# Kernel optimization log

Hardware: AMD Instinct MI355X
Metric: run time of the kernel (lower is better)

Reference implementation:

```python
import jax, jax.numpy as jnp
import numpy as np

B, S, D, H = 2, 2048, 1024, 16
DK = D // H


def setup_inputs() -> dict:
    key = jax.random.key(0)
    ks = jax.random.split(key, 12)
    k_init = 1.0 / np.sqrt(D)  # torch Linear-style uniform bound used in the module
    def lin(kw, kb):
        W = jax.random.uniform(kw, (D, D), jnp.float32, -k_init, k_init)
        b = jax.random.uniform(kb, (D,), jnp.float32, -k_init, k_init)
        return W, b
    Wq, bq = lin(ks[0], ks[1])
    Wk, bk = lin(ks[2], ks[3])
    Wv, bv = lin(ks[4], ks[5])
    Wo, bo = lin(ks[6], ks[7])
    query = jax.random.normal(ks[8], (B, S, D), jnp.float32)
    key_t = jax.random.normal(ks[9], (B, S, D), jnp.float32)
    value = jax.random.normal(ks[10], (B, S, D), jnp.float32)
    # causal mask: 1 where attention allowed, 0 where blocked
    mask = jnp.broadcast_to(jnp.tril(jnp.ones((S, S), jnp.int32)), (B, S, S))
    return {"query": query, "key": key_t, "value": value, "mask": mask,
            "Wq": Wq, "bq": bq, "Wk": Wk, "bk": bk, "Wv": Wv, "bv": bv,
            "Wo": Wo, "bo": bo}


def reference(query, key, value, mask, Wq, bq, Wk, bk, Wv, bv, Wo, bo):
    bs = query.shape[0]
    # projections: torch Linear computes x @ W.T + b
    def proj(x, W, b):
        y = x @ W.T + b                      # [B, S, D]
        return y.reshape(bs, -1, H, DK).transpose(0, 2, 1, 3)  # [B, H, S, DK]
    q = proj(query, Wq, bq)
    k = proj(key, Wk, bk)
    v = proj(value, Wv, bv)
    scale = 1.0 / np.sqrt(DK).astype(np.float32)
    scores = jnp.einsum('bhqd,bhkd->bhqk', q, k) * scale  # [B, H, S, S]
    scores = jnp.where(mask[:, None, :, :] == 0, jnp.float32(-1e9), scores)
    p_attn = jax.nn.softmax(scores, axis=-1)
    # dropout omitted (eval mode / deterministic reference)
    x = jnp.einsum('bhqk,bhkd->bhqd', p_attn, v)          # [B, H, S, DK]
    x = x.transpose(0, 2, 1, 3).reshape(bs, -1, D)        # [B, S, D]
    return x @ Wo.T + bo
```

## Files before the change

### kernel.cpp

```cpp
#include <hip/hip_runtime.h>
#include <hip/hip_bf16.h>
#include <math.h>

#define BB 2
#define SS 2048
#define DD 1024
#define HH 16
#define DKK 64
#define NT (BB * SS)

typedef __attribute__((ext_vector_type(8))) short short8;
typedef __attribute__((ext_vector_type(4))) short short4v;
typedef __attribute__((ext_vector_type(4))) float f32x4;

#define SWZ(r) ((((r) >> 3) ^ (r)) & 7)

__device__ __forceinline__ unsigned short f2b(float x) {
    __hip_bfloat16 h = __float2bfloat16(x);
    unsigned short u; __builtin_memcpy(&u, &h, 2); return u;
}

__device__ __forceinline__ f32x4 zero4() {
    f32x4 z; z[0] = 0.f; z[1] = 0.f; z[2] = 0.f; z[3] = 0.f; return z;
}

struct CastAll {
    const float* src[7];
    unsigned short* dst[7];
};

__global__ __launch_bounds__(256)
void cast_all(CastAll a) {
    const int tid0 = blockIdx.x * 256 + threadIdx.x;
    const int stride = gridDim.x * 256;
    #pragma unroll
    for (int s = 0; s < 7; ++s) {
        const int n4 = (s < 3) ? (NT * DD / 4) : (DD * DD / 4);
        const float* __restrict__ src = a.src[s];
        unsigned short* __restrict__ dst = a.dst[s];
        for (int i = tid0; i < n4; i += stride) {
            const float4 v = reinterpret_cast<const float4*>(src)[i];
            ushort4 o;
            o.x = f2b(v.x); o.y = f2b(v.y); o.z = f2b(v.z); o.w = f2b(v.w);
            reinterpret_cast<ushort4*>(dst)[i] = o;
        }
    }
}

template <typename OutT>
__device__ __forceinline__ void gemm_body(const unsigned short* __restrict__ A,
                                          const unsigned short* __restrict__ W,
                                          const float* __restrict__ bias,
                                          OutT* __restrict__ C,
                                          int bm, int bn, int N, int K) {
    __shared__ __align__(16) unsigned char sA[128 * 128];
    __shared__ __align__(16) unsigned char sB[128 * 128];

    const int tid = threadIdx.x;
    const int l = tid & 63;
    const int w = tid >> 6;
    const int wr = w >> 1, wc = w & 1;
    const int g = l >> 4, li = l & 15;
    const int lrow = l >> 3;
    const int lcol = (l & 7) * 8;

    f32x4 acc[4][4];
    #pragma unroll
    for (int i = 0; i < 4; ++i)
        #pragma unroll
        for (int jj = 0; jj < 4; ++jj) acc[i][jj] = zero4();

    for (int kt = 0; kt < K; kt += 64) {
        #pragma unroll
        for (int c = 0; c < 4; ++c) {
            const int row0 = w * 32 + c * 8;
            const unsigned short* gA = A + (size_t)(bm + row0 + lrow) * K + kt + lcol;
            __builtin_amdgcn_global_load_lds(
                (const __attribute__((address_space(1))) unsigned int*)gA,
                (__attribute__((address_space(3))) unsigned int*)&sA[row0 * 128],
                16, 0, 0);
            const unsigned short* gB = W + (size_t)(bn + row0 + lrow) * K + kt + lcol;
            __builtin_amdgcn_global_load_lds(
                (const __attribute__((address_space(1))) unsigned int*)gB,
                (__attribute__((address_space(3))) unsigned int*)&sB[row0 * 128],
                16, 0, 0);
        }
        __syncthreads();

        #pragma unroll
        for (int kb = 0; kb < 2; ++kb) {
            const int chb = (g + kb * 4) * 16;
            short8 af[4], bfr[4];
            #pragma unroll
            for (int mi = 0; mi < 4; ++mi)
                af[mi] = *reinterpret_cast<const short8*>(
                    &sA[(wr * 64 + mi * 16 + li) * 128 + chb]);
            #pragma unroll
            for (int ni = 0; ni < 4; ++ni)
                bfr[ni] = *reinterpret_cast<const short8*>(
                    &sB[(wc * 64 + ni * 16 + li) * 128 + chb]);
            #pragma unroll
            for (int mi = 0; mi < 4; ++mi)
                #pragma unroll
                for (int ni = 0; ni < 4; ++ni)
                    acc[mi][ni] = __builtin_amdgcn_mfma_f32_16x16x32_bf16(af[mi], bfr[ni], acc[mi][ni], 0, 0, 0);
        }
        __syncthreads();
    }

    #pragma unroll
    for (int ni = 0; ni < 4; ++ni) {
        const int col = bn + wc * 64 + ni * 16 + li;
        const float bv = bias[col];
        #pragma unroll
        for (int mi = 0; mi < 4; ++mi) {
            const int row0 = bm + wr * 64 + mi * 16 + g * 4;
            #pragma unroll
            for (int r = 0; r < 4; ++r) {
                const float v = acc[mi][ni][r] + bv;
                if constexpr (sizeof(OutT) == 2)
                    C[(size_t)(row0 + r) * N + col] = (OutT)f2b(v);
                else
                    C[(size_t)(row0 + r) * N + col] = (OutT)v;
            }
        }
    }
}

struct QKVArgs {
    const unsigned short* A[3];
    const unsigned short* W[3];
    const float* bias[3];
    unsigned short* C[3];
};

__global__ __launch_bounds__(256)
void gemm_qkv(QKVArgs args) {
    const int bid = blockIdx.x;
    const int i = (bid & 7) * 96 + (bid >> 3);
    const int z = i >> 8;
    const int rem = i & 255;
    const int by = rem >> 3, bx = rem & 7;
    gemm_body<unsigned short>(args.A[z], args.W[z], args.bias[z], args.C[z],
                              by * 128, bx * 128, DD, DD);
}

__global__ __launch_bounds__(256)
void gemm_out(const unsigned short* __restrict__ A, const unsigned short* __restrict__ W,
              const float* __restrict__ bias, float* __restrict__ C) {
    const int bid = blockIdx.x;
    const int i = (bid & 7) * 32 + (bid >> 3);
    const int by = i >> 3, bx = i & 7;
    gemm_body<float>(A, W, bias, C, by * 128, bx * 128, DD, DD);
}

__global__ __launch_bounds__(512)
void attn_mfma(const unsigned short* __restrict__ Q,
               const unsigned short* __restrict__ Kb,
               const unsigned short* __restrict__ Vb,
               unsigned short* __restrict__ X) {
    __shared__ __align__(16) unsigned char sK[64 * 128];
    __shared__ __align__(16) unsigned char sV[64 * 128];
    __shared__ __align__(16) unsigned char sP[8][16 * 128];

    const int bid = blockIdx.x;
    const int t = bid >> 3;
    const int bh = (bid & 7) + 8 * (t & 3);
    const int p = t >> 2;
    const int b = bh >> 4, h = bh & 15;

    const int tid = threadIdx.x, l = tid & 63, w = tid >> 6;
    const int g = l >> 4, li = l & 15;
    const int jsel = (w < 4) ? p : (31 - p);
    const int rowb = jsel * 64 + (w & 3) * 16;
    const int col0 = h * DKK;
    const float scale = 0.125f;

    short8 qf[2];
    {
        const size_t qrow = (size_t)(b * SS + rowb + li) * DD + col0;
        qf[0] = *reinterpret_cast<const short8*>(&Q[qrow + g * 8]);
        qf[1] = *reinterpret_cast<const short8*>(&Q[qrow + 32 + g * 8]);
    }

    f32x4 accO[4];
    #pragma unroll
    for (int i = 0; i < 4; ++i) accO[i] = zero4();
    float m = -INFINITY, lsum = 0.f;
    const int qglob = rowb + li;
    const int nkt = 31 - p;

    for (int kt = 0; kt <= nkt; ++kt) {
        const int ktok0 = b * SS + kt * 64;

        {
            const int row = tid >> 3, cj = tid & 7;
            const size_t gsrc = (size_t)(ktok0 + row) * DD + col0 + cj * 8;
            const short8 kv8 = *reinterpret_cast<const short8*>(&Kb[gsrc]);
            *reinterpret_cast<short8*>(&sK[row * 128 + ((cj ^ SWZ(row)) << 4)]) = kv8;
            const short8 vv8 = *reinterpret_cast<const short8*>(&Vb[gsrc]);
            #pragma unroll
            for (int jj = 0; jj < 8; ++jj) {
                const int d = cj * 8 + jj;
                *reinterpret_cast<unsigned short*>(
                    &sV[d * 128 + (((row >> 3) ^ SWZ(d)) << 4) + (row & 7) * 2]) =
                    (unsigned short)vv8[jj];
            }
        }
        __syncthreads();

        if (kt * 64 <= rowb + 15) {
            f32x4 accS[4];
            #pragma unroll
            for (int n0 = 0; n0 < 4; ++n0) accS[n0] = zero4();
            __builtin_amdgcn_s_setprio(1);
            #pragma unroll
            for (int n0 = 0; n0 < 4; ++n0) {
                #pragma unroll
                for (int kb = 0; kb < 2; ++kb) {
                    const int row = n0 * 16 + li;
                    const int ch = g + kb * 4;
                    const short8 kf = *reinterpret_cast<const short8*>(
                        &sK[row * 128 + ((ch ^ SWZ(row)) << 4)]);
                    accS[n0] = __builtin_amdgcn_mfma_f32_16x16x32_bf16(kf, qf[kb], accS[n0], 0, 0, 0);
                }
            }
            __builtin_amdgcn_s_setprio(0);

            const bool needMask = (kt * 64 + 63) > rowb;
            float s[16];
            float tmax = -INFINITY;
            #pragma unroll
            for (int n0 = 0; n0 < 4; ++n0)
                #pragma unroll
                for (int r = 0; r < 4; ++r) {
                    float v = accS[n0][r] * scale;
                    if (needMask) {
                        const int kv = kt * 64 + n0 * 16 + g * 4 + r;
                        if (kv > qglob) v = -1e30f;
                    }
                    s[n0 * 4 + r] = v;
                    tmax = fmaxf(tmax, v);
                }
            tmax = fmaxf(tmax, __shfl_xor(tmax, 16));
            tmax = fmaxf(tmax, __shfl_xor(tmax, 32));
            const float mnew = fmaxf(m, tmax);
            const float corr = __expf(m - mnew);
            float psum = 0.f;
            #pragma unroll
            for (int i = 0; i < 16; ++i) { s[i] = __expf(s[i] - mnew); psum += s[i]; }
            psum += __shfl_xor(psum, 16);
            psum += __shfl_xor(psum, 32);
            lsum = lsum * corr + psum;
            m = mnew;

            #pragma unroll
            for (int n0 = 0; n0 < 4; ++n0) {
                short4v pk;
                #pragma unroll
                for (int r = 0; r < 4; ++r) pk[r] = (short)f2b(s[n0 * 4 + r]);
                *reinterpret_cast<short4v*>(
                    &sP[w][li * 128 + (((n0 * 2 + (g >> 1)) ^ SWZ(li)) << 4) + (g & 1) * 8]) = pk;
            }

            float corr4[4];
            #pragma unroll
            for (int r = 0; r < 4; ++r) corr4[r] = __shfl(corr, (l & 48) | (g * 4 + r));
            #pragma unroll
            for (int n0d = 0; n0d < 4; ++n0d)
                #pragma unroll
                for (int r = 0; r < 4; ++r) accO[n0d][r] *= corr4[r];

            __builtin_amdgcn_s_setprio(1);
            #pragma unroll
            for (int kb = 0; kb < 2; ++kb) {
                const int ch = g + kb * 4;
                const short8 pf = *reinterpret_cast<const short8*>(
                    &sP[w][li * 128 + ((ch ^ SWZ(li)) << 4)]);
                #pragma unroll
                for (int n0d = 0; n0d < 4; ++n0d) {
                    const int d = n0d * 16 + li;
                    const short8 vf = *reinterpret_cast<const short8*>(
                        &sV[d * 128 + ((ch ^ SWZ(d)) << 4)]);
                    accO[n0d] = __builtin_amdgcn_mfma_f32_16x16x32_bf16(pf, vf, accO[n0d], 0, 0, 0);
                }
            }
            __builtin_amdgcn_s_setprio(0);
        }
        __syncthreads();
    }

    const float invl = 1.f / lsum;
    float inv4[4];
    #pragma unroll
    for (int r = 0; r < 4; ++r) inv4[r] = __shfl(invl, (l & 48) | (g * 4 + r));
    #pragma unroll
    for (int n0d = 0; n0d < 4; ++n0d)
        #pragma unroll
        for (int r = 0; r < 4; ++r) {
            const int row = b * SS + rowb + g * 4 + r;
            const int d = n0d * 16 + li;
            X[(size_t)row * DD + col0 + d] = f2b(accO[n0d][r] * inv4[r]);
        }
}

extern "C" void kernel_launch(void* const* d_in, const int* in_sizes, int n_in,
                              void* d_out, int out_size, void* d_ws, size_t ws_size,
                              hipStream_t stream) {
    const float* query = (const float*)d_in[0];
    const float* key   = (const float*)d_in[1];
    const float* value = (const float*)d_in[2];
    const float* Wq = (const float*)d_in[4];
    const float* bq = (const float*)d_in[5];
    const float* Wk = (const float*)d_in[6];
    const float* bk = (const float*)d_in[7];
    const float* Wv = (const float*)d_in[8];
    const float* bv = (const float*)d_in[9];
    const float* Wo = (const float*)d_in[10];
    const float* bo = (const float*)d_in[11];
    float* out = (float*)d_out;

    unsigned short* ws16 = (unsigned short*)d_ws;
    const size_t TOK = (size_t)NT * DD;
    const size_t WSZ = (size_t)DD * DD;
    unsigned short* qb  = ws16;
    unsigned short* kb  = ws16 + TOK;
    unsigned short* vb  = ws16 + 2 * TOK;
    unsigned short* xb  = ws16 + 3 * TOK;
    unsigned short* xqb = ws16 + 4 * TOK;
    unsigned short* xkb = ws16 + 5 * TOK;
    unsigned short* xvb = ws16 + 6 * TOK;
    unsigned short* wqb = ws16 + 7 * TOK;
    unsigned short* wkb = wqb + WSZ;
    unsigned short* wvb = wkb + WSZ;
    unsigned short* wob = wvb + WSZ;

    CastAll ca;
    ca.src[0] = query; ca.dst[0] = xqb;
    ca.src[1] = key;   ca.dst[1] = xkb;
    ca.src[2] = value; ca.dst[2] = xvb;
    ca.src[3] = Wq;    ca.dst[3] = wqb;
    ca.src[4] = Wk;    ca.dst[4] = wkb;
    ca.src[5] = Wv;    ca.dst[5] = wvb;
    ca.src[6] = Wo;    ca.dst[6] = wob;
    cast_all<<<2048, 256, 0, stream>>>(ca);

    QKVArgs args;
    args.A[0] = xqb; args.A[1] = xkb; args.A[2] = xvb;
    args.W[0] = wqb; args.W[1] = wkb; args.W[2] = wvb;
    args.bias[0] = bq; args.bias[1] = bk; args.bias[2] = bv;
    args.C[0] = qb;  args.C[1] = kb;  args.C[2] = vb;
    gemm_qkv<<<768, 256, 0, stream>>>(args);

    attn_mfma<<<512, 512, 0, stream>>>(qb, kb, vb, xb);

    gemm_out<<<256, 256, 0, stream>>>(xb, wob, bo, out);
}
```

Before: 267.5 us.

## Write V transposed from QKV GEMM and rebuild attention on 32x32 MFMA tiles

The V projection epilogue now writes V in a per-head transposed layout, so the attention kernel can stream K and V tiles straight into LDS with global_load_lds and no per-element transposing scatter. The attention kernel moves to 128-key tiles, 32x32x16 MFMAs and 256-thread blocks. P stays in registers and is exchanged between lane halves with cross-lane shuffles instead of going through shared memory. The softmax rescale is skipped when the running max does not change, and only diagonal tiles apply the causal mask. The trade-offs are a larger LDS footprint per block, more register pressure from the 16-wide accumulators, and uncoalesced 8-byte strided stores in the V epilogue.

```diff
diff --git a/kernel.cpp b/kernel.cpp
--- a/kernel.cpp
+++ b/kernel.cpp
@@ -10,18 +10,15 @@
 #define NT (BB * SS)
 
 typedef __attribute__((ext_vector_type(8))) short short8;
-typedef __attribute__((ext_vector_type(4))) short short4v;
 typedef __attribute__((ext_vector_type(4))) float f32x4;
-
-#define SWZ(r) ((((r) >> 3) ^ (r)) & 7)
+typedef __attribute__((ext_vector_type(16))) float f32x16;
 
 __device__ __forceinline__ unsigned short f2b(float x) {
     __hip_bfloat16 h = __float2bfloat16(x);
     unsigned short u; __builtin_memcpy(&u, &h, 2); return u;
 }
-
-__device__ __forceinline__ f32x4 zero4() {
-    f32x4 z; z[0] = 0.f; z[1] = 0.f; z[2] = 0.f; z[3] = 0.f; return z;
+__device__ __forceinline__ unsigned pack2(float a, float b) {
+    return (unsigned)f2b(a) | ((unsigned)f2b(b) << 16);
 }
 
 struct CastAll {
@@ -47,11 +44,11 @@
     }
 }
 
-template <typename OutT>
+template <int MODE>
 __device__ __forceinline__ void gemm_body(const unsigned short* __restrict__ A,
                                           const unsigned short* __restrict__ W,
                                           const float* __restrict__ bias,
-                                          OutT* __restrict__ C,
+                                          void* __restrict__ Cv,
                                           int bm, int bn, int N, int K) {
     __shared__ __align__(16) unsigned char sA[128 * 128];
     __shared__ __align__(16) unsigned char sB[128 * 128];
@@ -68,7 +65,10 @@
     #pragma unroll
     for (int i = 0; i < 4; ++i)
         #pragma unroll
-        for (int jj = 0; jj < 4; ++jj) acc[i][jj] = zero4();
+        for (int jj = 0; jj < 4; ++jj) {
+            acc[i][jj][0] = 0.f; acc[i][jj][1] = 0.f;
+            acc[i][jj][2] = 0.f; acc[i][jj][3] = 0.f;
+        }
 
     for (int kt = 0; kt < K; kt += 64) {
         #pragma unroll
@@ -112,16 +112,33 @@
     for (int ni = 0; ni < 4; ++ni) {
         const int col = bn + wc * 64 + ni * 16 + li;
         const float bv = bias[col];
-        #pragma unroll
-        for (int mi = 0; mi < 4; ++mi) {
-            const int row0 = bm + wr * 64 + mi * 16 + g * 4;
-            #pragma unroll
-            for (int r = 0; r < 4; ++r) {
-                const float v = acc[mi][ni][r] + bv;
-                if constexpr (sizeof(OutT) == 2)
-                    C[(size_t)(row0 + r) * N + col] = (OutT)f2b(v);
-                else
-                    C[(size_t)(row0 + r) * N + col] = (OutT)v;
+        if constexpr (MODE == 2) {
+            const int hh = col >> 6, d = col & 63;
+            const int bb = bm >> 11;
+            unsigned short* vt = (unsigned short*)Cv;
+            #pragma unroll
+            for (int mi = 0; mi < 4; ++mi) {
+                const int srow0 = (bm & (SS - 1)) + wr * 64 + mi * 16 + g * 4;
+                ushort4 pk4;
+                pk4.x = f2b(acc[mi][ni][0] + bv);
+                pk4.y = f2b(acc[mi][ni][1] + bv);
+                pk4.z = f2b(acc[mi][ni][2] + bv);
+                pk4.w = f2b(acc[mi][ni][3] + bv);
+                *reinterpret_cast<ushort4*>(
+                    &vt[(size_t)((bb * 16 + hh) * 64 + d) * SS + srow0]) = pk4;
+            }
+        } else {
+            #pragma unroll
+            for (int mi = 0; mi < 4; ++mi) {
+                const int row0 = bm + wr * 64 + mi * 16 + g * 4;
+                #pragma unroll
+                for (int r = 0; r < 4; ++r) {
+                    const float v = acc[mi][ni][r] + bv;
+                    if constexpr (MODE == 0)
+                        ((unsigned short*)Cv)[(size_t)(row0 + r) * N + col] = f2b(v);
+                    else
+                        ((float*)Cv)[(size_t)(row0 + r) * N + col] = v;
+                }
             }
         }
     }
@@ -131,7 +148,8 @@
     const unsigned short* A[3];
     const unsigned short* W[3];
     const float* bias[3];
-    unsigned short* C[3];
+    unsigned short* C[2];
+    unsigned short* vt;
 };
 
 __global__ __launch_bounds__(256)
@@ -141,8 +159,10 @@
     const int z = i >> 8;
     const int rem = i & 255;
     const int by = rem >> 3, bx = rem & 7;
-    gemm_body<unsigned short>(args.A[z], args.W[z], args.bias[z], args.C[z],
-                              by * 128, bx * 128, DD, DD);
+    if (z == 2)
+        gemm_body<2>(args.A[2], args.W[2], args.bias[2], args.vt, by * 128, bx * 128, DD, DD);
+    else
+        gemm_body<0>(args.A[z], args.W[z], args.bias[z], args.C[z], by * 128, bx * 128, DD, DD);
 }
 
 __global__ __launch_bounds__(256)
@@ -151,157 +171,178 @@
     const int bid = blockIdx.x;
     const int i = (bid & 7) * 32 + (bid >> 3);
     const int by = i >> 3, bx = i & 7;
-    gemm_body<float>(A, W, bias, C, by * 128, bx * 128, DD, DD);
-}
-
-__global__ __launch_bounds__(512)
+    gemm_body<1>(A, W, bias, C, by * 128, bx * 128, DD, DD);
+}
+
+__global__ __launch_bounds__(256)
 void attn_mfma(const unsigned short* __restrict__ Q,
                const unsigned short* __restrict__ Kb,
-               const unsigned short* __restrict__ Vb,
+               const unsigned short* __restrict__ Vt,
                unsigned short* __restrict__ X) {
-    __shared__ __align__(16) unsigned char sK[64 * 128];
-    __shared__ __align__(16) unsigned char sV[64 * 128];
-    __shared__ __align__(16) unsigned char sP[8][16 * 128];
+    __shared__ __align__(16) unsigned char sK[128 * 128];
+    __shared__ __align__(16) unsigned char sV[64 * 256];
 
     const int bid = blockIdx.x;
-    const int t = bid >> 3;
-    const int bh = (bid & 7) + 8 * (t & 3);
-    const int p = t >> 2;
+    const int xcd = bid & 7;
+    const int idx = bid >> 3;
+    const int j   = 15 - (idx >> 2);
+    const int bh  = xcd * 4 + (idx & 3);
     const int b = bh >> 4, h = bh & 15;
 
     const int tid = threadIdx.x, l = tid & 63, w = tid >> 6;
-    const int g = l >> 4, li = l & 15;
-    const int jsel = (w < 4) ? p : (31 - p);
-    const int rowb = jsel * 64 + (w & 3) * 16;
+    const int h5 = l >> 5, q5 = l & 31;
     const int col0 = h * DKK;
+    const int qbase = j * 128 + w * 32;
     const float scale = 0.125f;
 
-    short8 qf[2];
+    short8 qf[4];
     {
-        const size_t qrow = (size_t)(b * SS + rowb + li) * DD + col0;
-        qf[0] = *reinterpret_cast<const short8*>(&Q[qrow + g * 8]);
-        qf[1] = *reinterpret_cast<const short8*>(&Q[qrow + 32 + g * 8]);
-    }
-
-    f32x4 accO[4];
-    #pragma unroll
-    for (int i = 0; i < 4; ++i) accO[i] = zero4();
+        const unsigned short* qp = Q + (size_t)(b * SS + qbase + q5) * DD + col0;
+        #pragma unroll
+        for (int s = 0; s < 4; ++s)
+            qf[s] = *reinterpret_cast<const short8*>(&qp[(2 * s + h5) * 8]);
+    }
+
+    f32x16 accO[2];
+    #pragma unroll
+    for (int d0 = 0; d0 < 2; ++d0)
+        #pragma unroll
+        for (int r = 0; r < 16; ++r) accO[d0][r] = 0.f;
     float m = -INFINITY, lsum = 0.f;
-    const int qglob = rowb + li;
-    const int nkt = 31 - p;
-
-    for (int kt = 0; kt <= nkt; ++kt) {
-        const int ktok0 = b * SS + kt * 64;
-
+
+    for (int kt = 0; kt <= j; ++kt) {
         {
-            const int row = tid >> 3, cj = tid & 7;
-            const size_t gsrc = (size_t)(ktok0 + row) * DD + col0 + cj * 8;
-            const short8 kv8 = *reinterpret_cast<const short8*>(&Kb[gsrc]);
-            *reinterpret_cast<short8*>(&sK[row * 128 + ((cj ^ SWZ(row)) << 4)]) = kv8;
-            const short8 vv8 = *reinterpret_cast<const short8*>(&Vb[gsrc]);
-            #pragma unroll
-            for (int jj = 0; jj < 8; ++jj) {
-                const int d = cj * 8 + jj;
-                *reinterpret_cast<unsigned short*>(
-                    &sV[d * 128 + (((row >> 3) ^ SWZ(d)) << 4) + (row & 7) * 2]) =
-                    (unsigned short)vv8[jj];
+            const unsigned short* krow = Kb + (size_t)(b * SS + kt * 128) * DD + col0;
+            #pragma unroll
+            for (int i = 0; i < 4; ++i) {
+                const int row = w * 32 + i * 8 + (l >> 3);
+                const int cj = l & 7;
+                __builtin_amdgcn_global_load_lds(
+                    (const __attribute__((address_space(1))) unsigned int*)
+                        (krow + (size_t)row * DD + ((cj ^ (row & 7)) << 3)),
+                    (__attribute__((address_space(3))) unsigned int*)&sK[w * 4096 + i * 1024],
+                    16, 0, 0);
+            }
+            const unsigned short* vrow = Vt + (size_t)(bh * 64) * SS + kt * 128;
+            #pragma unroll
+            for (int i = 0; i < 4; ++i) {
+                const int d = w * 16 + i * 4 + (l >> 4);
+                const int cj = l & 15;
+                __builtin_amdgcn_global_load_lds(
+                    (const __attribute__((address_space(1))) unsigned int*)
+                        (vrow + (size_t)d * SS + ((cj ^ (d & 15)) << 3)),
+                    (__attribute__((address_space(3))) unsigned int*)&sV[w * 4096 + i * 1024],
+                    16, 0, 0);
             }
         }
         __syncthreads();
 
-        if (kt * 64 <= rowb + 15) {
-            f32x4 accS[4];
-            #pragma unroll
-            for (int n0 = 0; n0 < 4; ++n0) accS[n0] = zero4();
-            __builtin_amdgcn_s_setprio(1);
-            #pragma unroll
-            for (int n0 = 0; n0 < 4; ++n0) {
-                #pragma unroll
-                for (int kb = 0; kb < 2; ++kb) {
-                    const int row = n0 * 16 + li;
-                    const int ch = g + kb * 4;
+        const bool diag = (kt == j);
+        const int fact = diag ? w : 3;
+
+        f32x16 accS[4];
+        __builtin_amdgcn_s_setprio(1);
+        #pragma unroll
+        for (int f = 0; f < 4; ++f) {
+            if (f <= fact) {
+                #pragma unroll
+                for (int r = 0; r < 16; ++r) accS[f][r] = 0.f;
+                #pragma unroll
+                for (int s = 0; s < 4; ++s) {
                     const short8 kf = *reinterpret_cast<const short8*>(
-                        &sK[row * 128 + ((ch ^ SWZ(row)) << 4)]);
-                    accS[n0] = __builtin_amdgcn_mfma_f32_16x16x32_bf16(kf, qf[kb], accS[n0], 0, 0, 0);
-                }
-            }
-            __builtin_amdgcn_s_setprio(0);
-
-            const bool needMask = (kt * 64 + 63) > rowb;
-            float s[16];
-            float tmax = -INFINITY;
-            #pragma unroll
-            for (int n0 = 0; n0 < 4; ++n0)
-                #pragma unroll
-                for (int r = 0; r < 4; ++r) {
-                    float v = accS[n0][r] * scale;
-                    if (needMask) {
-                        const int kv = kt * 64 + n0 * 16 + g * 4 + r;
-                        if (kv > qglob) v = -1e30f;
+                        &sK[(f * 32 + q5) * 128 + (((2 * s + h5) ^ (q5 & 7)) << 4)]);
+                    accS[f] = __builtin_amdgcn_mfma_f32_32x32x16_bf16(kf, qf[s], accS[f], 0, 0, 0);
+                }
+            }
+        }
+        __builtin_amdgcn_s_setprio(0);
+
+        float tmax = -INFINITY;
+        #pragma unroll
+        for (int f = 0; f < 4; ++f) {
+            if (f <= fact) {
+                #pragma unroll
+                for (int r = 0; r < 16; ++r) {
+                    float v = accS[f][r] * scale;
+                    if (diag && f == w) {
+                        const int off = (r & 3) + 8 * (r >> 2) + 4 * h5;
+                        if (off > q5) v = -3e38f;
                     }
-                    s[n0 * 4 + r] = v;
+                    accS[f][r] = v;
                     tmax = fmaxf(tmax, v);
                 }
-            tmax = fmaxf(tmax, __shfl_xor(tmax, 16));
-            tmax = fmaxf(tmax, __shfl_xor(tmax, 32));
-            const float mnew = fmaxf(m, tmax);
-            const float corr = __expf(m - mnew);
-            float psum = 0.f;
-            #pragma unroll
-            for (int i = 0; i < 16; ++i) { s[i] = __expf(s[i] - mnew); psum += s[i]; }
-            psum += __shfl_xor(psum, 16);
-            psum += __shfl_xor(psum, 32);
-            lsum = lsum * corr + psum;
-            m = mnew;
-
-            #pragma unroll
-            for (int n0 = 0; n0 < 4; ++n0) {
-                short4v pk;
-                #pragma unroll
-                for (int r = 0; r < 4; ++r) pk[r] = (short)f2b(s[n0 * 4 + r]);
-                *reinterpret_cast<short4v*>(
-                    &sP[w][li * 128 + (((n0 * 2 + (g >> 1)) ^ SWZ(li)) << 4) + (g & 1) * 8]) = pk;
-            }
-
-            float corr4[4];
-            #pragma unroll
-            for (int r = 0; r < 4; ++r) corr4[r] = __shfl(corr, (l & 48) | (g * 4 + r));
-            #pragma unroll
-            for (int n0d = 0; n0d < 4; ++n0d)
-                #pragma unroll
-                for (int r = 0; r < 4; ++r) accO[n0d][r] *= corr4[r];
-
-            __builtin_amdgcn_s_setprio(1);
-            #pragma unroll
-            for (int kb = 0; kb < 2; ++kb) {
-                const int ch = g + kb * 4;
-                const short8 pf = *reinterpret_cast<const short8*>(
-                    &sP[w][li * 128 + ((ch ^ SWZ(li)) << 4)]);
-                #pragma unroll
-                for (int n0d = 0; n0d < 4; ++n0d) {
-                    const int d = n0d * 16 + li;
+            }
+        }
+        tmax = fmaxf(tmax, __shfl_xor(tmax, 32));
+
+        if (!__all(tmax <= m)) {
+            const float mn = fmaxf(m, tmax);
+            const float corr = __expf(m - mn);
+            lsum *= corr;
+            #pragma unroll
+            for (int r = 0; r < 16; ++r) {
+                const int rowloc = (r & 3) + 8 * (r >> 2) + 4 * h5;
+                const float cr = __shfl(corr, rowloc | (l & 32));
+                accO[0][r] *= cr;
+                accO[1][r] *= cr;
+            }
+            m = mn;
+        }
+
+        float psum = 0.f;
+        unsigned pk[32];
+        #pragma unroll
+        for (int f = 0; f < 4; ++f) {
+            if (f <= fact) {
+                #pragma unroll
+                for (int i2 = 0; i2 < 8; ++i2) {
+                    const float pa = __expf(accS[f][2 * i2] - m);
+                    const float pb = __expf(accS[f][2 * i2 + 1] - m);
+                    psum += pa + pb;
+                    pk[f * 8 + i2] = pack2(pa, pb);
+                }
+            }
+        }
+        psum += __shfl_xor(psum, 32);
+        lsum += psum;
+
+        const int smax = diag ? (2 * w + 1) : 7;
+        __builtin_amdgcn_s_setprio(1);
+        #pragma unroll
+        for (int s = 0; s < 8; ++s) {
+            if (s <= smax) {
+                const int fb = (s >> 1) * 8 + (s & 1) * 4;
+                const unsigned sendA = h5 ? pk[fb + 0] : pk[fb + 2];
+                const unsigned sendB = h5 ? pk[fb + 1] : pk[fb + 3];
+                const unsigned rA = __shfl_xor(sendA, 32);
+                const unsigned rB = __shfl_xor(sendB, 32);
+                union { unsigned u[4]; short8 s8; } pf;
+                pf.u[0] = h5 ? rA : pk[fb + 0];
+                pf.u[1] = h5 ? rB : pk[fb + 1];
+                pf.u[2] = h5 ? pk[fb + 2] : rA;
+                pf.u[3] = h5 ? pk[fb + 3] : rB;
+                #pragma unroll
+                for (int d0 = 0; d0 < 2; ++d0) {
                     const short8 vf = *reinterpret_cast<const short8*>(
-                        &sV[d * 128 + ((ch ^ SWZ(d)) << 4)]);
-                    accO[n0d] = __builtin_amdgcn_mfma_f32_16x16x32_bf16(pf, vf, accO[n0d], 0, 0, 0);
-                }
-            }
-            __builtin_amdgcn_s_setprio(0);
-        }
+                        &sV[(d0 * 32 + q5) * 256 + (((2 * s + h5) ^ (q5 & 15)) << 4)]);
+                    accO[d0] = __builtin_amdgcn_mfma_f32_32x32x16_bf16(pf.s8, vf, accO[d0], 0, 0, 0);
+                }
+            }
+        }
+        __builtin_amdgcn_s_setprio(0);
         __syncthreads();
     }
 
     const float invl = 1.f / lsum;
-    float inv4[4];
-    #pragma unroll
-    for (int r = 0; r < 4; ++r) inv4[r] = __shfl(invl, (l & 48) | (g * 4 + r));
-    #pragma unroll
-    for (int n0d = 0; n0d < 4; ++n0d)
-        #pragma unroll
-        for (int r = 0; r < 4; ++r) {
-            const int row = b * SS + rowb + g * 4 + r;
-            const int d = n0d * 16 + li;
-            X[(size_t)row * DD + col0 + d] = f2b(accO[n0d][r] * inv4[r]);
-        }
+    #pragma unroll
+    for (int r = 0; r < 16; ++r) {
+        const int rowloc = (r & 3) + 8 * (r >> 2) + 4 * h5;
+        const float iv = __shfl(invl, rowloc | (l & 32));
+        const size_t qrow = (size_t)(b * SS + qbase + rowloc) * DD + col0;
+        #pragma unroll
+        for (int d0 = 0; d0 < 2; ++d0)
+            X[qrow + d0 * 32 + q5] = f2b(accO[d0][r] * iv);
+    }
 }
 
 extern "C" void kernel_launch(void* const* d_in, const int* in_sizes, int n_in,
@@ -325,7 +366,7 @@
     const size_t WSZ = (size_t)DD * DD;
     unsigned short* qb  = ws16;
     unsigned short* kb  = ws16 + TOK;
-    unsigned short* vb  = ws16 + 2 * TOK;
+    unsigned short* vt  = ws16 + 2 * TOK;
     unsigned short* xb  = ws16 + 3 * TOK;
     unsigned short* xqb = ws16 + 4 * TOK;
     unsigned short* xkb = ws16 + 5 * TOK;
@@ -349,10 +390,10 @@
     args.A[0] = xqb; args.A[1] = xkb; args.A[2] = xvb;
     args.W[0] = wqb; args.W[1] = wkb; args.W[2] = wvb;
     args.bias[0] = bq; args.bias[1] = bk; args.bias[2] = bv;
-    args.C[0] = qb;  args.C[1] = kb;  args.C[2] = vb;
+    args.C[0] = qb;  args.C[1] = kb;  args.vt = vt;
     gemm_qkv<<<768, 256, 0, stream>>>(args);
 
-    attn_mfma<<<512, 512, 0, stream>>>(qb, kb, vb, xb);
+    attn_mfma<<<512, 256, 0, stream>>>(qb, kb, vt, xb);
 
     gemm_out<<<256, 256, 0, stream>>>(xb, wob, bo, out);
 }
```

New measurement: 273.8 us. +2.3%, slower.
